# Optimization experiments

Hardware: AMD Instinct MI355X
Metric: run time of the kernel (lower is better)

The kernel has to match this reference:

```python
import jax, jax.numpy as jnp
import numpy as np

B, S, IN, E, L, H, NC, NL = 4, 1000, 5, 256, 6, 8, 2, 50
DH = E // H


def _ln(x, g, b, eps=1e-5):
    m = jnp.mean(x, -1, keepdims=True)
    v = jnp.mean((x - m) ** 2, -1, keepdims=True)
    return (x - m) / jnp.sqrt(v + eps) * g + b


def _lin(x, w, b):
    return x @ w.T + b


def _ph_single(points, fw, db, law, lab):
    # points: (S, 2) -> (6,) persistence features
    scores = (points @ law.T + lab)[:, 0]
    wts = jax.nn.softmax(scores)
    _, idx = jax.lax.top_k(wts, NL)
    lm = points[idx]  # (NL, 2) landmarks
    d2 = jnp.sum((lm[:, None, :] - lm[None, :, :]) ** 2, -1)
    # safe sqrt (zero grad on zero diagonal) == torch.cdist
    dist = jnp.sqrt(jnp.where(d2 > 0, d2, 1.0)) * (d2 > 0)
    sd = dist * jnp.abs(fw[0, 0]) + db[0]
    K = jnp.exp(-sd)
    lap = jnp.diag(jnp.sum(K, 1)) - K
    ev, evec = jnp.linalg.eigh(lap)
    zm = (ev < 1e-6).astype(ev.dtype)
    n0 = jnp.sum(zm)
    s0 = jnp.sum(jnp.abs(ev) * zm)
    gap = ev[1] - ev[0]
    fied = jnp.std(evec[:, 1], ddof=1)  # torch.std is unbiased
    return jnp.stack([n0, s0, gap, fied, jnp.mean(ev[2:6]), jnp.std(ev[2:6], ddof=1)])


def _attn(x, pf, qw, qb, kw, kb, vw, vb, pw1, pb1, pw2, pb2, ow_, ob_):
    b, s, e = x.shape
    q = _lin(x, qw, qb).reshape(b, s, H, DH).transpose(0, 2, 1, 3)
    k = _lin(x, kw, kb).reshape(b, s, H, DH).transpose(0, 2, 1, 3)
    v = _lin(x, vw, vb).reshape(b, s, H, DH).transpose(0, 2, 1, 3)
    scores = jnp.einsum('bhqd,bhkd->bhqk', q, k) / DH ** 0.5
    tw = jax.nn.sigmoid(_lin(jax.nn.relu(_lin(pf, pw1, pb1)), pw2, pb2))  # (b, E)
    # expand + mean over embed dim collapses to one scalar per sample
    ts = jnp.mean(tw, -1).reshape(b, 1, 1, 1)
    aw = jax.nn.softmax(scores * ts, -1)
    out = jnp.einsum('bhqk,bhkd->bhqd', aw, v).transpose(0, 2, 1, 3).reshape(b, s, e)
    return _lin(out, ow_, ob_)


def _fwd(sequences, ph_fw, ph_db, ph_law, ph_lab,
         emb_w1, emb_b1, emb_w2, emb_b2, emb_ln_g, emb_ln_b, pos_enc,
         qw, qb, kw, kb, vw, vb, pe_w1, pe_b1, pe_w2, pe_b2, ow, ob,
         ln_g, ln_b, f_w1, f_b1, f_w2, f_b2,
         c_ln_g, c_ln_b, c_w1, c_b1, c_w2, c_b2):
    b, s, _ = sequences.shape
    t = jnp.broadcast_to(jnp.arange(s, dtype=sequences.dtype), (b, s))
    pc = jnp.stack([t, jnp.mean(sequences, 2)], 2)  # (b, s, 2) point clouds
    pf = jax.vmap(lambda p: _ph_single(p, ph_fw, ph_db, ph_law, ph_lab))(pc)  # (b, 6)
    x = _ln(_lin(jax.nn.relu(_lin(sequences, emb_w1, emb_b1)), emb_w2, emb_b2),
            emb_ln_g, emb_ln_b)
    x = x + pos_enc[:s][None]
    for l in range(L):
        att = _attn(x, pf, qw[l], qb[l], kw[l], kb[l], vw[l], vb[l],
                    pe_w1[l], pe_b1[l], pe_w2[l], pe_b2[l], ow[l], ob[l])
        x = _ln(x + att, ln_g[l], ln_b[l])  # NOTE: same LN reused twice, as in source
        ff = _lin(jax.nn.gelu(_lin(x, f_w1[l], f_b1[l]), approximate=False), f_w2[l], f_b2[l])
        x = _ln(x + ff, ln_g[l], ln_b[l])
    pwts = jax.nn.softmax(jnp.sum(x, -1), -1)[..., None]
    pooled = jnp.sum(x * pwts, 1)
    z = jax.nn.relu(_lin(_ln(pooled, c_ln_g, c_ln_b), c_w1, c_b1))
    return _lin(z, c_w2, c_b2)


def setup_inputs() -> dict:
    key = jax.random.key(0)
    ks = iter(jax.random.split(key, 64))

    def w(shape, fan_in):
        return jax.random.normal(next(ks), shape, jnp.float32) / np.sqrt(fan_in).astype(np.float32)

    z = lambda *sh: jnp.zeros(sh, jnp.float32)
    o = lambda *sh: jnp.ones(sh, jnp.float32)
    return dict(
        sequences=jax.random.normal(next(ks), (B, S, IN), jnp.float32),
        ph_fw=jnp.full((1, 1), 0.02, jnp.float32),  # small filtration scale keeps eigh well-conditioned
        ph_db=z(1),
        ph_law=w((1, 2), 2), ph_lab=z(1),
        emb_w1=w((E // 2, IN), IN), emb_b1=z(E // 2),
        emb_w2=w((E, E // 2), E // 2), emb_b2=z(E),
        emb_ln_g=o(E), emb_ln_b=z(E),
        pos_enc=jax.random.normal(next(ks), (1000, E), jnp.float32),
        qw=w((L, E, E), E), qb=z(L, E),
        kw=w((L, E, E), E), kb=z(L, E),
        vw=w((L, E, E), E), vb=z(L, E),
        pe_w1=w((L, E // 2, 6), 6), pe_b1=z(L, E // 2),
        pe_w2=w((L, E, E // 2), E // 2), pe_b2=z(L, E),
        ow=w((L, E, E), E), ob=z(L, E),
        ln_g=o(L, E), ln_b=z(L, E),
        f_w1=w((L, 4 * E, E), E), f_b1=z(L, 4 * E),
        f_w2=w((L, E, 4 * E), 4 * E), f_b2=z(L, E),
        c_ln_g=o(E), c_ln_b=z(E),
        c_w1=w((E // 2, E), E), c_b1=z(E // 2),
        c_w2=w((NC, E // 2), E // 2), c_b2=z(NC),
    )


def reference(sequences, ph_fw, ph_db, ph_law, ph_lab,
              emb_w1, emb_b1, emb_w2, emb_b2, emb_ln_g, emb_ln_b, pos_enc,
              qw, qb, kw, kb, vw, vb, pe_w1, pe_b1, pe_w2, pe_b2, ow, ob,
              ln_g, ln_b, f_w1, f_b1, f_w2, f_b2,
              c_ln_g, c_ln_b, c_w1, c_b1, c_w2, c_b2):
    return _fwd(sequences, ph_fw, ph_db, ph_law, ph_lab,
                emb_w1, emb_b1, emb_w2, emb_b2, emb_ln_g, emb_ln_b, pos_enc,
                qw, qb, kw, kb, vw, vb, pe_w1, pe_b1, pe_w2, pe_b2, ow, ob,
                ln_g, ln_b, f_w1, f_b1, f_w2, f_b2,
                c_ln_g, c_ln_b, c_w1, c_b1, c_w2, c_b2)
```

## Files before the change

kernel.cpp:

```cpp
#include <hip/hip_runtime.h>
#include <math.h>

constexpr int BB = 4;
constexpr int SS = 1000;
constexpr int INDIM = 5;
constexpr int EE = 256;
constexpr int LL = 6;
constexpr int HH = 8;
constexpr int DHH = 32;
constexpr int NLM = 50;
constexpr int FFD = 1024;

typedef short short8 __attribute__((ext_vector_type(8)));
typedef float f32x4 __attribute__((ext_vector_type(4)));
typedef unsigned short u16;
typedef unsigned long long u64;

__device__ inline u16 f2b(float f) {
  union { float f; unsigned u; } v; v.f = f;
  unsigned u = v.u;
  unsigned r = u + 0x7FFFu + ((u >> 16) & 1u);
  return (u16)(r >> 16);
}
__device__ inline float b2f(u16 b) {
  union { unsigned u; float f; } v; v.u = ((unsigned)b) << 16;
  return v.f;
}
__device__ inline short8 pack8(float4 a, float4 b) {
  short8 r;
  r[0] = (short)f2b(a.x); r[1] = (short)f2b(a.y);
  r[2] = (short)f2b(a.z); r[3] = (short)f2b(a.w);
  r[4] = (short)f2b(b.x); r[5] = (short)f2b(b.y);
  r[6] = (short)f2b(b.z); r[7] = (short)f2b(b.w);
  return r;
}

__device__ inline double wred_sum(double v) {
#pragma unroll
  for (int m = 1; m < 64; m <<= 1) v += __shfl_xor(v, m, 64);
  return v;
}
__device__ inline double wred_min(double v) {
#pragma unroll
  for (int m = 1; m < 64; m <<= 1) v = fmin(v, __shfl_xor(v, m, 64));
  return v;
}
__device__ inline double wred_max(double v) {
#pragma unroll
  for (int m = 1; m < 64; m <<= 1) v = fmax(v, __shfl_xor(v, m, 64));
  return v;
}
__device__ inline float wredf_sum(float v) {
#pragma unroll
  for (int m = 1; m < 64; m <<= 1) v += __shfl_xor(v, m, 64);
  return v;
}
__device__ inline int sgnbit(double x) {
  return (int)((unsigned long long)__double_as_longlong(x) >> 63);
}

struct PhS {
  double matA[NLM][51];
  union {
    u64 keys[1024];
    double vstore[NLM - 2][64];
  } u;
  double vbuf[64], wbuf[64];
  double pm[4][64];
  double dar[NLM], ear[NLM], e2a[NLM], tauA[NLM], evs[NLM];
  double gdl[NLM], gdd[NLM], gdu[NLM], gdu2[NLM], gz[NLM];
  float sm[SS];
  float lx[NLM], ly[NLM];
};
union FusedS { PhS ph; float h[4][128]; };

__global__ __launch_bounds__(256) void phembed_kernel(
    const float* __restrict__ seq, const float* __restrict__ ph_fw,
    const float* __restrict__ ph_db, const float* __restrict__ ph_law,
    const float* __restrict__ ph_lab, float* __restrict__ pf,
    const float* __restrict__ ew1, const float* __restrict__ eb1,
    const float* __restrict__ ew2, const float* __restrict__ eb2,
    const float* __restrict__ eg, const float* __restrict__ ebe,
    const float* __restrict__ pos, float* __restrict__ X, u16* __restrict__ Xb)
{
  __shared__ FusedS S;
  const int tid = threadIdx.x;
  const int lane = tid & 63, wid = tid >> 6;

  if (blockIdx.x < BB) {
    const int b = blockIdx.x;
    PhS& P = S.ph;
    const float law0 = ph_law[0], law1 = ph_law[1], labv = ph_lab[0];
    for (int s = tid; s < 1024; s += 256) {
      u64 key;
      if (s < SS) {
        const float* p = seq + ((size_t)b * SS + s) * INDIM;
        float m = (p[0] + p[1] + p[2] + p[3] + p[4]) * 0.2f;
        P.sm[s] = m;
        float sc = (float)s * law0 + m * law1 + labv;
        unsigned u = __float_as_uint(sc);
        unsigned asc = (u & 0x80000000u) ? ~u : (u | 0x80000000u);
        key = ((u64)(~asc) << 32) | (unsigned)s;
      } else {
        key = (0xFFFFFFFFull << 32) | (unsigned)s;
      }
      P.u.keys[s] = key;
    }
    __syncthreads();
    for (int k = 2; k <= 1024; k <<= 1) {
      for (int j = k >> 1; j > 0; j >>= 1) {
        for (int i = tid; i < 1024; i += 256) {
          int ixj = i ^ j;
          if (ixj > i) {
            u64 a = P.u.keys[i], c = P.u.keys[ixj];
            bool up = ((i & k) == 0);
            if ((a > c) == up) { P.u.keys[i] = c; P.u.keys[ixj] = a; }
          }
        }
        __syncthreads();
      }
    }
    if (tid < NLM) {
      int id = (int)(P.u.keys[tid] & 0xFFFFFFFFull);
      P.lx[tid] = (float)id;
      P.ly[tid] = P.sm[id];
    }
    __syncthreads();
    const float fwv = fabsf(ph_fw[0]);
    const float dbv = ph_db[0];
    for (int t = tid; t < NLM * NLM; t += 256) {
      int i = t / NLM, j = t % NLM;
      float dx = P.lx[i] - P.lx[j], dy = P.ly[i] - P.ly[j];
      float d2 = dx * dx + dy * dy;
      float dist = (d2 > 0.f) ? sqrtf(d2) : 0.f;
      float Kv = expf(-(dist * fwv + dbv));
      P.matA[i][j] = -(double)Kv;
    }
    __syncthreads();
    if (tid < NLM) {
      double rsum = 0.0;
      for (int j = 0; j < NLM; ++j) rsum -= P.matA[tid][j];
      P.matA[tid][tid] += rsum;
    }
    __syncthreads();

    for (int k = 0; k <= NLM - 3; ++k) {
      if (wid == 0) {
        double x = (lane > k && lane < NLM) ? P.matA[lane][k] : 0.0;
        double x0 = __shfl(x, k + 1, 64);
        double sigma = wred_sum((lane > k + 1) ? x * x : 0.0);
        double beta, tau, scale;
        if (sigma == 0.0) { beta = x0; tau = 0.0; scale = 0.0; }
        else {
          double nrm = sqrt(x0 * x0 + sigma);
          beta = (x0 >= 0.0) ? -nrm : nrm;
          tau = (beta - x0) / beta;
          scale = 1.0 / (x0 - beta);
        }
        double v = (lane == k + 1) ? 1.0 : ((lane > k + 1 && lane < NLM) ? x * scale : 0.0);
        P.vbuf[lane] = v;
        P.u.vstore[k][lane] = v;
        if (lane == 0) { P.ear[k] = beta; P.tauA[k] = tau; }
      }
      __syncthreads();
      {
        double partial = 0.0;
        if (lane < NLM) {
          int j0 = wid * 13;
#pragma unroll
          for (int jj = 0; jj < 13; ++jj) {
            int j = j0 + jj;
            if (j < NLM) partial += P.matA[lane][j] * P.vbuf[j];
          }
        }
        P.pm[wid][lane] = partial;
      }
      __syncthreads();
      if (wid == 0) {
        double tau = P.tauA[k];
        double p = 0.0;
        if (lane < NLM)
          p = (P.pm[0][lane] + P.pm[1][lane] + P.pm[2][lane] + P.pm[3][lane]) * tau;
        double vr = P.vbuf[lane];
        double dotvp = wred_sum(vr * p);
        double w = p - 0.5 * tau * dotvp * vr;
        P.wbuf[lane] = (lane < NLM) ? w : 0.0;
      }
      __syncthreads();
      if (lane < NLM) {
        double vr = P.vbuf[lane], wr = P.wbuf[lane];
        int j0 = wid * 13;
#pragma unroll
        for (int jj = 0; jj < 13; ++jj) {
          int j = j0 + jj;
          if (j < NLM) P.matA[lane][j] -= vr * P.wbuf[j] + wr * P.vbuf[j];
        }
      }
      __syncthreads();
    }
    if (tid < NLM) P.dar[tid] = P.matA[tid][tid];
    if (tid == 0) P.ear[NLM - 2] = P.matA[NLM - 1][NLM - 2];
    __syncthreads();
    if (tid < NLM - 1) P.e2a[tid] = P.ear[tid] * P.ear[tid];
    __syncthreads();

    double lo_i = 1e300, hi_i = -1e300;
    if (lane < NLM) {
      double rl = (lane > 0) ? fabs(P.ear[lane - 1]) : 0.0;
      double rr = (lane < NLM - 1) ? fabs(P.ear[lane]) : 0.0;
      double dd = P.dar[lane];
      lo_i = dd - rl - rr;
      hi_i = dd + rl + rr;
    }
    double glo = wred_min(lo_i), ghi = wred_max(hi_i);

    if (tid < 100) {
      const int e = tid >> 1;
      const int side = tid & 1;
      const int need = e + 1;
      double lo = glo, hi = ghi;
      for (int it = 0; it < 24; ++it) {
        double third = (hi - lo) * (1.0 / 3.0);
        double x1 = lo + third, x2 = hi - third;
        double x = side ? x2 : x1;
        double p = P.dar[0] - x, q = 1.0;
        int c = sgnbit(p);
#pragma unroll 7
        for (int i = 1; i < NLM; ++i) {
          double n = (P.dar[i] - x) * p - P.e2a[i - 1] * q;
          if (n == 0.0) n = sgnbit(p) ? -1e-300 : 1e-300;
          c += (sgnbit(n) != sgnbit(p));
          long long an = __double_as_longlong(n) & 0x7fffffffffffffffLL;
          long long ap = __double_as_longlong(p) & 0x7fffffffffffffffLL;
          int E = (int)((an > ap ? an : ap) >> 52);
          int se = 2046 - E; se = se < 1 ? 1 : (se > 2045 ? 2045 : se);
          double s = __longlong_as_double((long long)se << 52);
          q = p * s; p = n * s;
        }
        int cp = __shfl_xor(c, 1, 64);
        int c1 = side ? cp : c;
        int c2 = side ? c : cp;
        if (c1 >= need) hi = x1;
        else if (c2 >= need) { lo = x1; hi = x2; }
        else lo = x2;
      }
      if (side == 0) P.evs[e] = 0.5 * (lo + hi);
    }
    __syncthreads();

    if (wid != 0) return;

    if (lane == 0) {
      double shift = P.evs[1];
      unsigned rs = 12345u;
      for (int i = 0; i < NLM; ++i) {
        rs = rs * 1103515245u + 12345u;
        P.gz[i] = ((double)((rs >> 8) & 0xFFFF)) / 65536.0 - 0.5;
      }
      for (int iter = 0; iter < 2; ++iter) {
        for (int i = 0; i < NLM; ++i) P.gdd[i] = P.dar[i] - shift;
        for (int i = 0; i < NLM - 1; ++i) { P.gdl[i] = P.ear[i]; P.gdu[i] = P.ear[i]; }
        for (int i = 0; i < NLM - 1; ++i) {
          if (fabs(P.gdd[i]) >= fabs(P.gdl[i])) {
            if (P.gdd[i] == 0.0) P.gdd[i] = 1e-280;
            double fact = P.gdl[i] / P.gdd[i];
            P.gdd[i + 1] -= fact * P.gdu[i];
            P.gz[i + 1] -= fact * P.gz[i];
            if (i < NLM - 2) P.gdu2[i] = 0.0;
          } else {
            double fact = P.gdd[i] / P.gdl[i];
            P.gdd[i] = P.gdl[i];
            double tmp = P.gdd[i + 1];
            P.gdd[i + 1] = P.gdu[i] - fact * tmp;
            if (i < NLM - 2) { P.gdu2[i] = P.gdu[i + 1]; P.gdu[i + 1] = -fact * P.gdu2[i]; }
            P.gdu[i] = tmp;
            double tz = P.gz[i]; P.gz[i] = P.gz[i + 1]; P.gz[i + 1] = tz - fact * P.gz[i];
          }
        }
        if (P.gdd[NLM - 1] == 0.0) P.gdd[NLM - 1] = 1e-280;
        P.gz[NLM - 1] /= P.gdd[NLM - 1];
        P.gz[NLM - 2] = (P.gz[NLM - 2] - P.gdu[NLM - 2] * P.gz[NLM - 1]) / P.gdd[NLM - 2];
        for (int i = NLM - 3; i >= 0; --i)
          P.gz[i] = (P.gz[i] - P.gdu[i] * P.gz[i + 1] - P.gdu2[i] * P.gz[i + 2]) / P.gdd[i];
        double nr = 0.0;
        for (int i = 0; i < NLM; ++i) nr += P.gz[i] * P.gz[i];
        nr = sqrt(nr);
        for (int i = 0; i < NLM; ++i) P.gz[i] /= nr;
      }
    }
    __builtin_amdgcn_wave_barrier();
    double fied = (lane < NLM) ? P.gz[lane] : 0.0;
    for (int k = NLM - 3; k >= 0; --k) {
      double v = P.u.vstore[k][lane];
      double dot = wred_sum(v * fied);
      fied -= P.tauA[k] * dot * v;
    }

    double myev = (lane < NLM) ? P.evs[lane] : 1e300;
    bool inR = (lane < NLM);
    double n0 = wred_sum((inR && myev < 1e-6) ? 1.0 : 0.0);
    double s0 = wred_sum((inR && myev < 1e-6) ? fabs(myev) : 0.0);
    double e0 = P.evs[0], e1 = P.evs[1];
    double e2 = P.evs[2], e3 = P.evs[3], e4 = P.evs[4], e5 = P.evs[5];
    double gap = e1 - e0;
    double m4 = (e2 + e3 + e4 + e5) * 0.25;
    double v4 = ((e2 - m4) * (e2 - m4) + (e3 - m4) * (e3 - m4) +
                 (e4 - m4) * (e4 - m4) + (e5 - m4) * (e5 - m4)) / 3.0;
    double fmean = wred_sum(inR ? fied : 0.0) / NLM;
    double fd = inR ? (fied - fmean) : 0.0;
    double fvar = wred_sum(fd * fd) / (NLM - 1);
    if (lane == 0) {
      float* o = pf + b * 6;
      o[0] = (float)n0;
      o[1] = (float)s0;
      o[2] = (float)gap;
      o[3] = (float)sqrt(fvar);
      o[4] = (float)m4;
      o[5] = (float)sqrt(v4);
    }
    return;
  }

  const int row = (blockIdx.x - BB) * 4 + wid;
  const int s = row % SS;
  float* hb = S.h[wid];
  float sv0, sv1, sv2, sv3, sv4;
  {
    const float* p = seq + (size_t)row * INDIM;
    sv0 = p[0]; sv1 = p[1]; sv2 = p[2]; sv3 = p[3]; sv4 = p[4];
  }
#pragma unroll
  for (int half = 0; half < 2; ++half) {
    int j = lane + half * 64;
    const float* w = ew1 + j * INDIM;
    float a = eb1[j] + w[0] * sv0 + w[1] * sv1 + w[2] * sv2 + w[3] * sv3 + w[4] * sv4;
    hb[j] = fmaxf(a, 0.f);
  }
  __builtin_amdgcn_wave_barrier();
  float o4[4];
#pragma unroll
  for (int q = 0; q < 4; ++q) {
    int e = lane * 4 + q;
    const float* w = ew2 + (size_t)e * 128;
    float a0 = 0.f, a1 = 0.f;
    for (int i = 0; i < 128; i += 8) {
      float4 wa = *(const float4*)(w + i);
      float4 wb = *(const float4*)(w + i + 4);
      a0 += wa.x * hb[i] + wa.y * hb[i + 1] + wa.z * hb[i + 2] + wa.w * hb[i + 3];
      a1 += wb.x * hb[i + 4] + wb.y * hb[i + 5] + wb.z * hb[i + 6] + wb.w * hb[i + 7];
    }
    o4[q] = eb2[e] + a0 + a1;
  }
  float ssum = o4[0] + o4[1] + o4[2] + o4[3];
  ssum = wredf_sum(ssum);
  float mean = ssum * (1.f / EE);
  float d0 = o4[0] - mean, d1 = o4[1] - mean, d2 = o4[2] - mean, d3 = o4[3] - mean;
  float qsum = d0 * d0 + d1 * d1 + d2 * d2 + d3 * d3;
  qsum = wredf_sum(qsum);
  float inv = rsqrtf(qsum * (1.f / EE) + 1e-5f);
  float4 gv = *(const float4*)(eg + lane * 4);
  float4 bv = *(const float4*)(ebe + lane * 4);
  float4 pv = *(const float4*)(pos + (size_t)s * EE + lane * 4);
  float4 outv = make_float4(d0 * inv * gv.x + bv.x + pv.x,
                            d1 * inv * gv.y + bv.y + pv.y,
                            d2 * inv * gv.z + bv.z + pv.z,
                            d3 * inv * gv.w + bv.w + pv.w);
  *(float4*)(X + (size_t)row * EE + lane * 4) = outv;
  *(ushort4*)(Xb + (size_t)row * EE + lane * 4) =
      make_ushort4(f2b(outv.x), f2b(outv.y), f2b(outv.z), f2b(outv.w));
}

__global__ __launch_bounds__(256) void temp_kernel(
    const float* __restrict__ pf, const float* __restrict__ w1, const float* __restrict__ b1,
    const float* __restrict__ w2, const float* __restrict__ b2, float* __restrict__ ts)
{
  const int l = blockIdx.x / BB, b = blockIdx.x % BB, tid = threadIdx.x;
  __shared__ float pfl[6];
  __shared__ float h[128];
  __shared__ float red[256];
  if (tid < 6) pfl[tid] = pf[b * 6 + tid];
  __syncthreads();
  if (tid < 128) {
    const float* w = w1 + ((size_t)l * 128 + tid) * 6;
    float a = b1[(size_t)l * 128 + tid];
#pragma unroll
    for (int i = 0; i < 6; ++i) a += w[i] * pfl[i];
    h[tid] = fmaxf(a, 0.f);
  }
  __syncthreads();
  const float* w = w2 + ((size_t)l * EE + tid) * 128;
  float a = b2[(size_t)l * EE + tid];
  for (int i = 0; i < 128; ++i) a += w[i] * h[i];
  float sg = 1.f / (1.f + expf(-a));
  red[tid] = sg; __syncthreads();
  for (int wd = 128; wd > 0; wd >>= 1) { if (tid < wd) red[tid] += red[tid + wd]; __syncthreads(); }
  if (tid == 0) ts[l * BB + b] = red[0] * (1.f / EE);
}

template <int AF32, int ACT>
__global__ __launch_bounds__(256) void gemm_bt(
    const void* __restrict__ Aptr,
    const float* __restrict__ W0, const float* __restrict__ W1, const float* __restrict__ W2,
    const float* __restrict__ bb0, const float* __restrict__ bb1, const float* __restrict__ bb2,
    u16* __restrict__ C0, u16* __restrict__ C1, u16* __restrict__ C2,
    int M, int N, int K)
{
  const int z = blockIdx.z;
  const float* W = (z == 0) ? W0 : (z == 1) ? W1 : W2;
  const float* bias = (z == 0) ? bb0 : (z == 1) ? bb1 : bb2;
  u16* C = (z == 0) ? C0 : (z == 1) ? C1 : C2;
  __shared__ __align__(16) u16 As[2][64][40];
  __shared__ __align__(16) u16 Bs[2][64][40];
  const int m0 = blockIdx.x * 64, n0 = blockIdx.y * 64;
  const int tid = threadIdx.x;
  const int lane = tid & 63, wave = tid >> 6;
  const int wm = wave >> 1, wn = wave & 1;
  const int l15 = lane & 15, l4 = lane >> 4;
  const int srow = tid >> 2, scg = (tid & 3) * 8;

  const float* Af = (const float*)Aptr;
  const u16* Ab = (const u16*)Aptr;

  f32x4 acc[2][2];
#pragma unroll
  for (int i = 0; i < 2; ++i)
#pragma unroll
    for (int j = 0; j < 2; ++j) acc[i][j] = (f32x4){0.f, 0.f, 0.f, 0.f};

  short8 areg, breg;
  auto do_load = [&](int t) {
    int kk = t * 32 + scg;
    if (AF32) {
      float4 a0 = *(const float4*)(Af + (size_t)(m0 + srow) * K + kk);
      float4 a1 = *(const float4*)(Af + (size_t)(m0 + srow) * K + kk + 4);
      areg = pack8(a0, a1);
    } else {
      areg = *(const short8*)(Ab + (size_t)(m0 + srow) * K + kk);
    }
    float4 b0 = *(const float4*)(W + (size_t)(n0 + srow) * K + kk);
    float4 b1 = *(const float4*)(W + (size_t)(n0 + srow) * K + kk + 4);
    breg = pack8(b0, b1);
  };
  auto do_write = [&](int buf) {
    *(short8*)&As[buf][srow][scg] = areg;
    *(short8*)&Bs[buf][srow][scg] = breg;
  };

  const int NT = K / 32;
  do_load(0);
  do_write(0);
  __syncthreads();
  for (int t = 0; t < NT; ++t) {
    const int cur = t & 1;
    if (t + 1 < NT) do_load(t + 1);
    short8 af0 = *(const short8*)&As[cur][wm * 32 + l15][l4 * 8];
    short8 af1 = *(const short8*)&As[cur][wm * 32 + 16 + l15][l4 * 8];
    short8 bf0 = *(const short8*)&Bs[cur][wn * 32 + l15][l4 * 8];
    short8 bf1 = *(const short8*)&Bs[cur][wn * 32 + 16 + l15][l4 * 8];
    acc[0][0] = __builtin_amdgcn_mfma_f32_16x16x32_bf16(af0, bf0, acc[0][0], 0, 0, 0);
    acc[0][1] = __builtin_amdgcn_mfma_f32_16x16x32_bf16(af0, bf1, acc[0][1], 0, 0, 0);
    acc[1][0] = __builtin_amdgcn_mfma_f32_16x16x32_bf16(af1, bf0, acc[1][0], 0, 0, 0);
    acc[1][1] = __builtin_amdgcn_mfma_f32_16x16x32_bf16(af1, bf1, acc[1][1], 0, 0, 0);
    if (t + 1 < NT) do_write(cur ^ 1);
    __syncthreads();
  }
#pragma unroll
  for (int nf = 0; nf < 2; ++nf) {
    int col = n0 + wn * 32 + nf * 16 + l15;
    float bv = bias[col];
#pragma unroll
    for (int mf = 0; mf < 2; ++mf) {
#pragma unroll
      for (int r = 0; r < 4; ++r) {
        int row = m0 + wm * 32 + mf * 16 + l4 * 4 + r;
        if (row < M) {
          float v = acc[mf][nf][r] + bv;
          if (ACT == 1) v = 0.5f * v * (1.f + erff(v * 0.70710678118654752440f));
          C[(size_t)row * N + col] = f2b(v);
        }
      }
    }
  }
}

template <int K>
__global__ __launch_bounds__(256) void gemm_ln16(
    const u16* __restrict__ A, const float* __restrict__ W,
    const float* __restrict__ bias, const float* __restrict__ g,
    const float* __restrict__ be, float* __restrict__ X, u16* __restrict__ Xb)
{
  __shared__ __align__(16) u16 As[2][16][40];
  __shared__ __align__(16) u16 Bs[2][256][40];
  __shared__ float wsum[4][16], wsq[4][16];
  const int m0 = blockIdx.x * 16;
  const int tid = threadIdx.x;
  const int lane = tid & 63, wave = tid >> 6;
  const int l15 = lane & 15, l4 = lane >> 4;
  const int srow = tid >> 2, scg = (tid & 3) * 8;

  f32x4 acc[4];
#pragma unroll
  for (int i = 0; i < 4; ++i) acc[i] = (f32x4){0.f, 0.f, 0.f, 0.f};

  short8 areg, breg[4];
  auto do_load = [&](int t) {
    int kk = t * 32;
    if (tid < 64) {
      int arow = tid >> 2, acg = (tid & 3) * 8;
      areg = *(const short8*)(A + (size_t)(m0 + arow) * K + kk + acg);
    }
#pragma unroll
    for (int q = 0; q < 4; ++q) {
      float4 b0 = *(const float4*)(W + (size_t)(q * 64 + srow) * K + kk + scg);
      float4 b1 = *(const float4*)(W + (size_t)(q * 64 + srow) * K + kk + scg + 4);
      breg[q] = pack8(b0, b1);
    }
  };
  auto do_write = [&](int buf) {
    if (tid < 64) {
      int arow = tid >> 2, acg = (tid & 3) * 8;
      *(short8*)&As[buf][arow][acg] = areg;
    }
#pragma unroll
    for (int q = 0; q < 4; ++q) *(short8*)&Bs[buf][q * 64 + srow][scg] = breg[q];
  };

  const int NT = K / 32;
  do_load(0);
  do_write(0);
  __syncthreads();
  for (int t = 0; t < NT; ++t) {
    const int cur = t & 1;
    if (t + 1 < NT) do_load(t + 1);
    short8 af = *(const short8*)&As[cur][l15][l4 * 8];
#pragma unroll
    for (int nf = 0; nf < 4; ++nf) {
      short8 bf = *(const short8*)&Bs[cur][wave * 64 + nf * 16 + l15][l4 * 8];
      acc[nf] = __builtin_amdgcn_mfma_f32_16x16x32_bf16(af, bf, acc[nf], 0, 0, 0);
    }
    if (t + 1 < NT) do_write(cur ^ 1);
    __syncthreads();
  }

#pragma unroll
  for (int nf = 0; nf < 4; ++nf) {
    int col = wave * 64 + nf * 16 + l15;
    float bv = bias[col];
#pragma unroll
    for (int r = 0; r < 4; ++r) {
      int row = m0 + l4 * 4 + r;
      acc[nf][r] += bv + X[(size_t)row * EE + col];
    }
  }
#pragma unroll
  for (int r = 0; r < 4; ++r) {
    float s = acc[0][r] + acc[1][r] + acc[2][r] + acc[3][r];
    float q = acc[0][r] * acc[0][r] + acc[1][r] * acc[1][r] +
              acc[2][r] * acc[2][r] + acc[3][r] * acc[3][r];
#pragma unroll
    for (int m = 1; m < 16; m <<= 1) {
      s += __shfl_xor(s, m, 64);
      q += __shfl_xor(q, m, 64);
    }
    if (l15 == 0) {
      wsum[wave][l4 * 4 + r] = s;
      wsq[wave][l4 * 4 + r] = q;
    }
  }
  __syncthreads();
#pragma unroll
  for (int r = 0; r < 4; ++r) {
    int rl = l4 * 4 + r;
    float Ssum = wsum[0][rl] + wsum[1][rl] + wsum[2][rl] + wsum[3][rl];
    float Qsum = wsq[0][rl] + wsq[1][rl] + wsq[2][rl] + wsq[3][rl];
    float mean = Ssum * (1.f / EE);
    float var = Qsum * (1.f / EE) - mean * mean;
    float inv = rsqrtf(var + 1e-5f);
    int row = m0 + rl;
#pragma unroll
    for (int nf = 0; nf < 4; ++nf) {
      int col = wave * 64 + nf * 16 + l15;
      float o = (acc[nf][r] - mean) * inv * g[col] + be[col];
      X[(size_t)row * EE + col] = o;
      Xb[(size_t)row * EE + col] = f2b(o);
    }
  }
}

__global__ __launch_bounds__(256) void attn_mfma(
    const u16* __restrict__ Qm, const u16* __restrict__ Km, const u16* __restrict__ Vm,
    const float* __restrict__ ts, u16* __restrict__ Om, int l)
{
  const int qt = blockIdx.x, h = blockIdx.y, b = blockIdx.z;
  const int tid = threadIdx.x;
  const int lane = tid & 63, wave = tid >> 6;
  const int l15 = lane & 15, l4 = lane >> 4;
  const float scale = ts[l * BB + b] * 0.17677669529663688110f;
  __shared__ __align__(16) u16 Ks[64][40];
  __shared__ __align__(16) u16 Vt[32][72];
  __shared__ __align__(16) u16 Pw[4][16][72];
  const int q0 = qt * 64 + wave * 16;
  const int srow = tid >> 2, scg = (tid & 3) * 8;

  short8 qf = {0, 0, 0, 0, 0, 0, 0, 0};
  {
    int qrow = q0 + l15;
    if (qrow < SS)
      qf = *(const short8*)(Qm + ((size_t)(b * SS + qrow)) * EE + h * DHH + l4 * 8);
  }

  float mrun[4] = {-INFINITY, -INFINITY, -INFINITY, -INFINITY};
  float lrun[4] = {0.f, 0.f, 0.f, 0.f};
  f32x4 Oacc[2];
  Oacc[0] = (f32x4){0.f, 0.f, 0.f, 0.f};
  Oacc[1] = (f32x4){0.f, 0.f, 0.f, 0.f};

  for (int k0 = 0; k0 < SS; k0 += 64) {
    int kn = SS - k0; if (kn > 64) kn = 64;
    __syncthreads();
    {
      short8 kv8 = {0, 0, 0, 0, 0, 0, 0, 0};
      if (srow < kn)
        kv8 = *(const short8*)(Km + ((size_t)(b * SS + k0 + srow)) * EE + h * DHH + scg);
      *(short8*)&Ks[srow][scg] = kv8;
    }
    {
      int d = tid & 31, kb = tid >> 5;
      u16 uu[8];
#pragma unroll
      for (int i = 0; i < 8; ++i) {
        int kv = kb * 8 + i;
        uu[i] = (kv < kn) ? Vm[((size_t)(b * SS + k0 + kv)) * EE + h * DHH + d] : (u16)0;
      }
      *(ushort4*)(&Vt[d][kb * 8])     = make_ushort4(uu[0], uu[1], uu[2], uu[3]);
      *(ushort4*)(&Vt[d][kb * 8 + 4]) = make_ushort4(uu[4], uu[5], uu[6], uu[7]);
    }
    __syncthreads();

    f32x4 sa[4];
#pragma unroll
    for (int nf = 0; nf < 4; ++nf) {
      short8 kf = *(const short8*)(&Ks[nf * 16 + l15][l4 * 8]);
      f32x4 zz = (f32x4){0.f, 0.f, 0.f, 0.f};
      sa[nf] = __builtin_amdgcn_mfma_f32_16x16x32_bf16(qf, kf, zz, 0, 0, 0);
    }
#pragma unroll
    for (int nf = 0; nf < 4; ++nf) {
      bool valid = (nf * 16 + l15) < kn;
#pragma unroll
      for (int r = 0; r < 4; ++r)
        sa[nf][r] = valid ? sa[nf][r] * scale : -INFINITY;
    }
    float pv[4][4];
#pragma unroll
    for (int r = 0; r < 4; ++r) {
      float tmax = fmaxf(fmaxf(sa[0][r], sa[1][r]), fmaxf(sa[2][r], sa[3][r]));
#pragma unroll
      for (int m = 1; m < 16; m <<= 1) tmax = fmaxf(tmax, __shfl_xor(tmax, m, 64));
      float mnew = fmaxf(mrun[r], tmax);
      float fac = expf(mrun[r] - mnew);
      float rsum = 0.f;
#pragma unroll
      for (int nf = 0; nf < 4; ++nf) {
        float p = expf(sa[nf][r] - mnew);
        pv[nf][r] = p;
        rsum += p;
      }
#pragma unroll
      for (int m = 1; m < 16; m <<= 1) rsum += __shfl_xor(rsum, m, 64);
      lrun[r] = lrun[r] * fac + rsum;
      mrun[r] = mnew;
      Oacc[0][r] *= fac;
      Oacc[1][r] *= fac;
    }
#pragma unroll
    for (int nf = 0; nf < 4; ++nf)
#pragma unroll
      for (int r = 0; r < 4; ++r)
        Pw[wave][l4 * 4 + r][nf * 16 + l15] = f2b(pv[nf][r]);
    asm volatile("s_waitcnt lgkmcnt(0)" ::: "memory");
    __builtin_amdgcn_sched_barrier(0);
#pragma unroll
    for (int ka = 0; ka < 2; ++ka) {
      short8 pa = *(const short8*)(&Pw[wave][l15][ka * 32 + l4 * 8]);
#pragma unroll
      for (int df = 0; df < 2; ++df) {
        short8 vf = *(const short8*)(&Vt[df * 16 + l15][ka * 32 + l4 * 8]);
        Oacc[df] = __builtin_amdgcn_mfma_f32_16x16x32_bf16(pa, vf, Oacc[df], 0, 0, 0);
      }
    }
  }
#pragma unroll
  for (int df = 0; df < 2; ++df)
#pragma unroll
    for (int r = 0; r < 4; ++r) {
      int qrow = q0 + l4 * 4 + r;
      if (qrow < SS)
        Om[((size_t)(b * SS + qrow)) * EE + h * DHH + df * 16 + l15] = f2b(Oacc[df][r] / lrun[r]);
    }
}

__global__ __launch_bounds__(256) void final_kernel(
    const float* __restrict__ X, const float* __restrict__ g, const float* __restrict__ be,
    const float* __restrict__ w1, const float* __restrict__ b1,
    const float* __restrict__ w2, const float* __restrict__ b2,
    float* __restrict__ out)
{
  const int b = blockIdx.x, tid = threadIdx.x;
  __shared__ float rs[SS];
  __shared__ float red[256];
  __shared__ float pooled[EE];
  __shared__ float h[128];
  for (int s = tid; s < SS; s += 256) {
    const float* xr = X + ((size_t)(b * SS + s)) * EE;
    float a = 0.f;
    for (int e = 0; e < EE; ++e) a += xr[e];
    rs[s] = a;
  }
  __syncthreads();
  float mx = -INFINITY;
  for (int s = tid; s < SS; s += 256) mx = fmaxf(mx, rs[s]);
  red[tid] = mx; __syncthreads();
  for (int w = 128; w > 0; w >>= 1) { if (tid < w) red[tid] = fmaxf(red[tid], red[tid + w]); __syncthreads(); }
  mx = red[0]; __syncthreads();
  float sme = 0.f;
  for (int s = tid; s < SS; s += 256) { float e2 = expf(rs[s] - mx); rs[s] = e2; sme += e2; }
  red[tid] = sme; __syncthreads();
  for (int w = 128; w > 0; w >>= 1) { if (tid < w) red[tid] += red[tid + w]; __syncthreads(); }
  float tot = red[0]; __syncthreads();
  float acc = 0.f;
  for (int s = 0; s < SS; ++s) acc += X[((size_t)(b * SS + s)) * EE + tid] * rs[s];
  acc /= tot;
  red[tid] = acc; __syncthreads();
  for (int w = 128; w > 0; w >>= 1) { if (tid < w) red[tid] += red[tid + w]; __syncthreads(); }
  float mean = red[0] * (1.f / EE); __syncthreads();
  float d = acc - mean;
  red[tid] = d * d; __syncthreads();
  for (int w = 128; w > 0; w >>= 1) { if (tid < w) red[tid] += red[tid + w]; __syncthreads(); }
  float var = red[0] * (1.f / EE);
  pooled[tid] = d * rsqrtf(var + 1e-5f) * g[tid] + be[tid];
  __syncthreads();
  if (tid < 128) {
    const float* w = w1 + (size_t)tid * EE;
    float a = b1[tid];
    for (int e = 0; e < EE; ++e) a += w[e] * pooled[e];
    h[tid] = fmaxf(a, 0.f);
  }
  __syncthreads();
  if (tid < 2) {
    const float* w = w2 + (size_t)tid * 128;
    float a = b2[tid];
    for (int j = 0; j < 128; ++j) a += w[j] * h[j];
    out[b * 2 + tid] = a;
  }
}

extern "C" void kernel_launch(void* const* d_in, const int* in_sizes, int n_in,
                              void* d_out, int out_size, void* d_ws, size_t ws_size,
                              hipStream_t stream) {
  (void)in_sizes; (void)n_in; (void)out_size; (void)ws_size;
  const float* seq    = (const float*)d_in[0];
  const float* ph_fw  = (const float*)d_in[1];
  const float* ph_db  = (const float*)d_in[2];
  const float* ph_law = (const float*)d_in[3];
  const float* ph_lab = (const float*)d_in[4];
  const float* emb_w1 = (const float*)d_in[5];
  const float* emb_b1 = (const float*)d_in[6];
  const float* emb_w2 = (const float*)d_in[7];
  const float* emb_b2 = (const float*)d_in[8];
  const float* eln_g  = (const float*)d_in[9];
  const float* eln_b  = (const float*)d_in[10];
  const float* pos    = (const float*)d_in[11];
  const float* qw     = (const float*)d_in[12];
  const float* qb     = (const float*)d_in[13];
  const float* kw     = (const float*)d_in[14];
  const float* kb     = (const float*)d_in[15];
  const float* vw     = (const float*)d_in[16];
  const float* vb     = (const float*)d_in[17];
  const float* pw1    = (const float*)d_in[18];
  const float* pb1    = (const float*)d_in[19];
  const float* pw2    = (const float*)d_in[20];
  const float* pb2    = (const float*)d_in[21];
  const float* ow     = (const float*)d_in[22];
  const float* obv    = (const float*)d_in[23];
  const float* lng    = (const float*)d_in[24];
  const float* lnb    = (const float*)d_in[25];
  const float* fw1    = (const float*)d_in[26];
  const float* fb1    = (const float*)d_in[27];
  const float* fw2    = (const float*)d_in[28];
  const float* fb2    = (const float*)d_in[29];
  const float* clng   = (const float*)d_in[30];
  const float* clnb   = (const float*)d_in[31];
  const float* cw1    = (const float*)d_in[32];
  const float* cb1    = (const float*)d_in[33];
  const float* cw2    = (const float*)d_in[34];
  const float* cb2    = (const float*)d_in[35];

  float* ws  = (float*)d_ws;
  float* pf  = ws;
  float* tsv = ws + 32;
  const size_t SL = (size_t)4096 * 256;
  float* X = ws + 256;
  u16* Xb   = (u16*)(X + SL);
  u16* Qb   = Xb + SL;
  u16* Kb   = Qb + SL;
  u16* Vb   = Kb + SL;
  u16* ATTb = Vb + SL;
  u16* HIDb = ATTb + SL;
  const int M = BB * SS;

  phembed_kernel<<<BB + M / 4, 256, 0, stream>>>(
      seq, ph_fw, ph_db, ph_law, ph_lab, pf,
      emb_w1, emb_b1, emb_w2, emb_b2, eln_g, eln_b, pos, X, Xb);
  temp_kernel<<<LL * BB, 256, 0, stream>>>(pf, pw1, pb1, pw2, pb2, tsv);

  const int GM = 63;
  const int GL = 250;
  for (int l = 0; l < LL; ++l) {
    const size_t wo = (size_t)l * EE * EE;
    gemm_bt<0, 0><<<dim3(GM, EE / 64, 3), 256, 0, stream>>>(
        Xb, qw + wo, kw + wo, vw + wo, qb + l * EE, kb + l * EE, vb + l * EE,
        Qb, Kb, Vb, M, EE, EE);
    attn_mfma<<<dim3(16, HH, BB), 256, 0, stream>>>(Qb, Kb, Vb, tsv, ATTb, l);
    gemm_ln16<EE><<<GL, 256, 0, stream>>>(
        ATTb, ow + wo, obv + l * EE, lng + l * EE, lnb + l * EE, X, Xb);
    gemm_bt<0, 1><<<dim3(GM, FFD / 64, 1), 256, 0, stream>>>(
        Xb, fw1 + (size_t)l * FFD * EE, fw1 + (size_t)l * FFD * EE, fw1 + (size_t)l * FFD * EE,
        fb1 + (size_t)l * FFD, fb1 + (size_t)l * FFD, fb1 + (size_t)l * FFD,
        HIDb, HIDb, HIDb, M, FFD, EE);
    gemm_ln16<FFD><<<GL, 256, 0, stream>>>(
        HIDb, fw2 + (size_t)l * EE * FFD, fb2 + l * EE, lng + l * EE, lnb + l * EE, X, Xb);
  }

  final_kernel<<<BB, 256, 0, stream>>>(X, clng, clnb, cw1, cb1, cw2, cb2, (float*)d_out);
}
```

Before: 985.0 us.

## Enlarge GEMM M-tile to 128, trim Householder loops, vectorize final row sums

The bf16 GEMM now computes 128x64 tiles, with each wave holding four M-fragments, so every converted weight tile is reused across twice as many rows and the grid shrinks from 63 to 32 row blocks. The Householder tridiagonalization restricts its matrix-vector product and rank-2 update to the active trailing columns, splitting them evenly across the four waves instead of sweeping all 50 columns. The final pooling kernel computes per-row sums with one wave per row, using float4 loads and a wave reduction, in place of a serial loop per thread. The larger tile leaves fewer blocks to fill the GPU and reads rows past M=4000 in the last block (up to 4095), which depends on the workspace being large enough.

```diff
diff --git a/kernel.cpp b/kernel.cpp
--- a/kernel.cpp
+++ b/kernel.cpp
@@ -145,6 +145,7 @@
     __syncthreads();
 
     for (int k = 0; k <= NLM - 3; ++k) {
+      const int m = NLM - 1 - k;
       if (wid == 0) {
         double x = (lane > k && lane < NLM) ? P.matA[lane][k] : 0.0;
         double x0 = __shfl(x, k + 1, 64);
@@ -164,15 +165,12 @@
       }
       __syncthreads();
       {
+        int chunk = (m + 3) >> 2;
+        int j0 = k + 1 + wid * chunk;
+        int j1 = j0 + chunk; if (j1 > NLM) j1 = NLM;
         double partial = 0.0;
-        if (lane < NLM) {
-          int j0 = wid * 13;
-#pragma unroll
-          for (int jj = 0; jj < 13; ++jj) {
-            int j = j0 + jj;
-            if (j < NLM) partial += P.matA[lane][j] * P.vbuf[j];
-          }
-        }
+        if (lane < NLM)
+          for (int j = j0; j < j1; ++j) partial += P.matA[lane][j] * P.vbuf[j];
         P.pm[wid][lane] = partial;
       }
       __syncthreads();
@@ -187,13 +185,14 @@
         P.wbuf[lane] = (lane < NLM) ? w : 0.0;
       }
       __syncthreads();
-      if (lane < NLM) {
-        double vr = P.vbuf[lane], wr = P.wbuf[lane];
-        int j0 = wid * 13;
-#pragma unroll
-        for (int jj = 0; jj < 13; ++jj) {
-          int j = j0 + jj;
-          if (j < NLM) P.matA[lane][j] -= vr * P.wbuf[j] + wr * P.vbuf[j];
+      {
+        int chunk = (m + 4) >> 2;
+        int j0 = k + wid * chunk;
+        int j1 = j0 + chunk; if (j1 > NLM) j1 = NLM;
+        if (lane < NLM) {
+          double vr = P.vbuf[lane], wr = P.wbuf[lane];
+          for (int j = j0; j < j1; ++j)
+            P.matA[lane][j] -= vr * P.wbuf[j] + wr * P.vbuf[j];
         }
       }
       __syncthreads();
@@ -397,9 +396,9 @@
   if (tid == 0) ts[l * BB + b] = red[0] * (1.f / EE);
 }
 
-template <int AF32, int ACT>
+template <int ACT>
 __global__ __launch_bounds__(256) void gemm_bt(
-    const void* __restrict__ Aptr,
+    const u16* __restrict__ Ab,
     const float* __restrict__ W0, const float* __restrict__ W1, const float* __restrict__ W2,
     const float* __restrict__ bb0, const float* __restrict__ bb1, const float* __restrict__ bb2,
     u16* __restrict__ C0, u16* __restrict__ C1, u16* __restrict__ C2,
@@ -409,40 +408,33 @@
   const float* W = (z == 0) ? W0 : (z == 1) ? W1 : W2;
   const float* bias = (z == 0) ? bb0 : (z == 1) ? bb1 : bb2;
   u16* C = (z == 0) ? C0 : (z == 1) ? C1 : C2;
-  __shared__ __align__(16) u16 As[2][64][40];
+  __shared__ __align__(16) u16 As[2][128][40];
   __shared__ __align__(16) u16 Bs[2][64][40];
-  const int m0 = blockIdx.x * 64, n0 = blockIdx.y * 64;
+  const int m0 = blockIdx.x * 128, n0 = blockIdx.y * 64;
   const int tid = threadIdx.x;
   const int lane = tid & 63, wave = tid >> 6;
   const int wm = wave >> 1, wn = wave & 1;
   const int l15 = lane & 15, l4 = lane >> 4;
   const int srow = tid >> 2, scg = (tid & 3) * 8;
 
-  const float* Af = (const float*)Aptr;
-  const u16* Ab = (const u16*)Aptr;
-
-  f32x4 acc[2][2];
-#pragma unroll
-  for (int i = 0; i < 2; ++i)
+  f32x4 acc[4][2];
+#pragma unroll
+  for (int i = 0; i < 4; ++i)
 #pragma unroll
     for (int j = 0; j < 2; ++j) acc[i][j] = (f32x4){0.f, 0.f, 0.f, 0.f};
 
-  short8 areg, breg;
+  short8 areg0, areg1, breg;
   auto do_load = [&](int t) {
     int kk = t * 32 + scg;
-    if (AF32) {
-      float4 a0 = *(const float4*)(Af + (size_t)(m0 + srow) * K + kk);
-      float4 a1 = *(const float4*)(Af + (size_t)(m0 + srow) * K + kk + 4);
-      areg = pack8(a0, a1);
-    } else {
-      areg = *(const short8*)(Ab + (size_t)(m0 + srow) * K + kk);
-    }
+    areg0 = *(const short8*)(Ab + (size_t)(m0 + srow) * K + kk);
+    areg1 = *(const short8*)(Ab + (size_t)(m0 + srow + 64) * K + kk);
     float4 b0 = *(const float4*)(W + (size_t)(n0 + srow) * K + kk);
     float4 b1 = *(const float4*)(W + (size_t)(n0 + srow) * K + kk + 4);
     breg = pack8(b0, b1);
   };
   auto do_write = [&](int buf) {
-    *(short8*)&As[buf][srow][scg] = areg;
+    *(short8*)&As[buf][srow][scg] = areg0;
+    *(short8*)&As[buf][srow + 64][scg] = areg1;
     *(short8*)&Bs[buf][srow][scg] = breg;
   };
 
@@ -453,14 +445,14 @@
   for (int t = 0; t < NT; ++t) {
     const int cur = t & 1;
     if (t + 1 < NT) do_load(t + 1);
-    short8 af0 = *(const short8*)&As[cur][wm * 32 + l15][l4 * 8];
-    short8 af1 = *(const short8*)&As[cur][wm * 32 + 16 + l15][l4 * 8];
     short8 bf0 = *(const short8*)&Bs[cur][wn * 32 + l15][l4 * 8];
     short8 bf1 = *(const short8*)&Bs[cur][wn * 32 + 16 + l15][l4 * 8];
-    acc[0][0] = __builtin_amdgcn_mfma_f32_16x16x32_bf16(af0, bf0, acc[0][0], 0, 0, 0);
-    acc[0][1] = __builtin_amdgcn_mfma_f32_16x16x32_bf16(af0, bf1, acc[0][1], 0, 0, 0);
-    acc[1][0] = __builtin_amdgcn_mfma_f32_16x16x32_bf16(af1, bf0, acc[1][0], 0, 0, 0);
-    acc[1][1] = __builtin_amdgcn_mfma_f32_16x16x32_bf16(af1, bf1, acc[1][1], 0, 0, 0);
+#pragma unroll
+    for (int mf = 0; mf < 4; ++mf) {
+      short8 af = *(const short8*)&As[cur][wm * 64 + mf * 16 + l15][l4 * 8];
+      acc[mf][0] = __builtin_amdgcn_mfma_f32_16x16x32_bf16(af, bf0, acc[mf][0], 0, 0, 0);
+      acc[mf][1] = __builtin_amdgcn_mfma_f32_16x16x32_bf16(af, bf1, acc[mf][1], 0, 0, 0);
+    }
     if (t + 1 < NT) do_write(cur ^ 1);
     __syncthreads();
   }
@@ -469,10 +461,10 @@
     int col = n0 + wn * 32 + nf * 16 + l15;
     float bv = bias[col];
 #pragma unroll
-    for (int mf = 0; mf < 2; ++mf) {
+    for (int mf = 0; mf < 4; ++mf) {
 #pragma unroll
       for (int r = 0; r < 4; ++r) {
-        int row = m0 + wm * 32 + mf * 16 + l4 * 4 + r;
+        int row = m0 + wm * 64 + mf * 16 + l4 * 4 + r;
         if (row < M) {
           float v = acc[mf][nf][r] + bv;
           if (ACT == 1) v = 0.5f * v * (1.f + erff(v * 0.70710678118654752440f));
@@ -707,15 +699,17 @@
     float* __restrict__ out)
 {
   const int b = blockIdx.x, tid = threadIdx.x;
+  const int lane = tid & 63, wid = tid >> 6;
   __shared__ float rs[SS];
   __shared__ float red[256];
   __shared__ float pooled[EE];
   __shared__ float h[128];
-  for (int s = tid; s < SS; s += 256) {
+  for (int s = wid; s < SS; s += 4) {
     const float* xr = X + ((size_t)(b * SS + s)) * EE;
-    float a = 0.f;
-    for (int e = 0; e < EE; ++e) a += xr[e];
-    rs[s] = a;
+    float4 v = *(const float4*)(xr + lane * 4);
+    float a = v.x + v.y + v.z + v.w;
+    a = wredf_sum(a);
+    if (lane == 0) rs[s] = a;
   }
   __syncthreads();
   float mx = -INFINITY;
@@ -814,17 +808,17 @@
       emb_w1, emb_b1, emb_w2, emb_b2, eln_g, eln_b, pos, X, Xb);
   temp_kernel<<<LL * BB, 256, 0, stream>>>(pf, pw1, pb1, pw2, pb2, tsv);
 
-  const int GM = 63;
+  const int GM = 32;
   const int GL = 250;
   for (int l = 0; l < LL; ++l) {
     const size_t wo = (size_t)l * EE * EE;
-    gemm_bt<0, 0><<<dim3(GM, EE / 64, 3), 256, 0, stream>>>(
+    gemm_bt<0><<<dim3(GM, EE / 64, 3), 256, 0, stream>>>(
         Xb, qw + wo, kw + wo, vw + wo, qb + l * EE, kb + l * EE, vb + l * EE,
         Qb, Kb, Vb, M, EE, EE);
     attn_mfma<<<dim3(16, HH, BB), 256, 0, stream>>>(Qb, Kb, Vb, tsv, ATTb, l);
     gemm_ln16<EE><<<GL, 256, 0, stream>>>(
         ATTb, ow + wo, obv + l * EE, lng + l * EE, lnb + l * EE, X, Xb);
-    gemm_bt<0, 1><<<dim3(GM, FFD / 64, 1), 256, 0, stream>>>(
+    gemm_bt<1><<<dim3(GM, FFD / 64, 1), 256, 0, stream>>>(
         Xb, fw1 + (size_t)l * FFD * EE, fw1 + (size_t)l * FFD * EE, fw1 + (size_t)l * FFD * EE,
         fb1 + (size_t)l * FFD, fb1 + (size_t)l * FFD, fb1 + (size_t)l * FFD,
         HIDb, HIDb, HIDb, M, FFD, EE);
```

After: 1.071 ms. 1.09x slower.
